# Kernel optimization log

Hardware: AMD Instinct MI355X
Metric: run time of the kernel (lower is better)

## Reference

```python
import jax, jax.numpy as jnp
import numpy as np

N_NODES = 50000
N_EDGES = 800000
D_IN, D_HID, D_OUT = 96, 96, 48


def _gcn_conv(x, src, dst, W, b, num_nodes):
    """PyG GCNConv: h = x @ W; out[dst] += norm * h[src]; out += b.
    Symmetric normalization deg^{-1/2}[src] * deg^{-1/2}[dst], self-loops included
    (src/dst already contain self-loops)."""
    h = x @ W  # [N, d_out]
    deg = jax.ops.segment_sum(jnp.ones_like(dst, dtype=h.dtype), dst,
                              num_segments=num_nodes)  # in-degree incl. self-loop
    dinv = jnp.where(deg > 0, jax.lax.rsqrt(deg), 0.0)
    norm = dinv[src] * dinv[dst]  # [E+N]
    msgs = h[src] * norm[:, None]  # gather + scale (the memory-bound part)
    out = jax.ops.segment_sum(msgs, dst, num_segments=num_nodes)  # scatter-add
    return out + b


def setup_inputs() -> dict:
    key = jax.random.key(0)
    k1, k2, k3, k4 = jax.random.split(key, 4)
    x = jax.random.normal(k1, (N_NODES, D_IN), dtype=jnp.float32)
    edge_index = jax.random.randint(k2, (2, N_EDGES), 0, N_NODES, dtype=jnp.int64)
    # Glorot-ish init for weights, zero bias (matches GCNConv defaults)
    W1 = jax.random.normal(k3, (D_IN, D_HID), dtype=jnp.float32) / np.sqrt(D_IN)
    b1 = jnp.zeros((D_HID,), dtype=jnp.float32)
    W2 = jax.random.normal(k4, (D_HID, D_OUT), dtype=jnp.float32) / np.sqrt(D_HID)
    b2 = jnp.zeros((D_OUT,), dtype=jnp.float32)
    return {"x": x, "edge_index": edge_index, "W1": W1, "b1": b1, "W2": W2, "b2": b2}


def reference(x, edge_index, W1, b1, W2, b2):
    num_nodes = x.shape[0]
    loops = jnp.arange(num_nodes, dtype=edge_index.dtype)
    src = jnp.concatenate([edge_index[0], loops])  # add self-loops
    dst = jnp.concatenate([edge_index[1], loops])
    h = _gcn_conv(x, src, dst, W1, b1, num_nodes)
    h = jax.nn.relu(h)
    # dropout p=0.5 is identity in eval mode (self.training=False)
    out = _gcn_conv(h, src, dst, W2, b2, num_nodes)
    return out
```

## Files before the change

### kernel.cpp

```cpp
#include <hip/hip_runtime.h>
#include <hip/hip_bf16.h>


constexpr int NN = 50000;
constexpr int NE = 800000;
constexpr int DI = 96;
constexpr int DH = 96;
constexpr int DO = 48;

constexpr int BK_SHIFT = 6;
constexpr int NBK      = (NN + 63) >> 6;
constexpr int BK_CAP   = 2048;

constexpr int NCHUNK = 256;
constexpr int CH     = (NE + NCHUNK - 1) / NCHUNK;

typedef unsigned short us8 __attribute__((ext_vector_type(8)));

__device__ __forceinline__ float bf2f(unsigned short u) {
    return __uint_as_float(((unsigned int)u) << 16);
}
__device__ __forceinline__ unsigned short f2bf(float f) {
    __hip_bfloat16 b = __float2bfloat16(f);
    return *reinterpret_cast<unsigned short*>(&b);
}


__global__ __launch_bounds__(256) void k_hist(const int* __restrict__ dst,
                                              int* __restrict__ C, int e) {
    __shared__ int hist[NBK];
    for (int i = threadIdx.x; i < NBK; i += 256) hist[i] = 0;
    __syncthreads();
    const int blk = blockIdx.x;
    const int beg = blk * CH, end = min(beg + CH, e);
    for (int i = beg + threadIdx.x; i < end; i += 256)
        atomicAdd(&hist[dst[i] >> BK_SHIFT], 1);
    __syncthreads();
    for (int b = threadIdx.x; b < NBK; b += 256)
        C[b * NCHUNK + blk] = hist[b];
}

__global__ __launch_bounds__(256) void k_rowscan(int* __restrict__ C,
                                                 int* __restrict__ totals,
                                                 int* __restrict__ row_ptr) {
    if (blockIdx.x == 0 && threadIdx.x == 0) row_ptr[NN] = NE;
    const int w    = threadIdx.x >> 6;
    const int lane = threadIdx.x & 63;
    const int r    = blockIdx.x * 4 + w;
    if (r >= NBK) return;
    int* row = C + r * NCHUNK;
    int v[4], s[4];
#pragma unroll
    for (int q = 0; q < 4; ++q) { v[q] = row[q * 64 + lane]; s[q] = v[q]; }
#pragma unroll
    for (int off = 1; off < 64; off <<= 1) {
#pragma unroll
        for (int q = 0; q < 4; ++q) {
            int y = __shfl_up(s[q], off);
            if (lane >= off) s[q] += y;
        }
    }
    int c0 = __shfl(s[0], 63);
    int c1 = __shfl(s[1], 63);
    int c2 = __shfl(s[2], 63);
    s[1] += c0;
    s[2] += c0 + c1;
    s[3] += c0 + c1 + c2;
#pragma unroll
    for (int q = 0; q < 4; ++q) row[q * 64 + lane] = s[q] - v[q];
    if (lane == 63) totals[r] = s[3];
}

__global__ __launch_bounds__(256) void k_scatter(const int* __restrict__ src,
                                                 const int* __restrict__ dst,
                                                 const int* __restrict__ C,
                                                 const int* __restrict__ totals,
                                                 int* __restrict__ bk_ptr,
                                                 unsigned* __restrict__ ebuf, int e) {
    __shared__ int bkL[NBK + 1];
    __shared__ int part[256];
    __shared__ int cur[NBK];
    const int t = threadIdx.x;

    int v[4];
    int s = 0;
    const int base = t * 4;
#pragma unroll
    for (int i = 0; i < 4; ++i) {
        int idx = base + i;
        v[i] = (idx < NBK) ? totals[idx] : 0;
        s += v[i];
    }
    part[t] = s;
    __syncthreads();
#pragma unroll
    for (int off = 1; off < 256; off <<= 1) {
        int x = part[t];
        int a = (t >= off) ? part[t - off] : 0;
        __syncthreads();
        part[t] = x + a;
        __syncthreads();
    }
    int run = part[t] - s;
#pragma unroll
    for (int i = 0; i < 4; ++i) {
        int idx = base + i;
        if (idx <= NBK) bkL[idx] = run;
        run += v[i];
    }
    __syncthreads();

    const int blk = blockIdx.x;
    for (int b = t; b < NBK; b += 256) cur[b] = bkL[b] + C[b * NCHUNK + blk];
    if (blk == 0)
        for (int i = t; i <= NBK; i += 256) bk_ptr[i] = bkL[i];
    __syncthreads();

    const int beg = blk * CH, end = min(beg + CH, e);
    for (int i = beg + t; i < end; i += 256) {
        int d = dst[i];
        int b = d >> BK_SHIFT;
        int pos = atomicAdd(&cur[b], 1);
        ebuf[pos] = ((unsigned)(d & 63) << 16) | (unsigned)src[i];
    }
}

__global__ __launch_bounds__(256) void k_bsort(const unsigned* __restrict__ ebuf,
                                               const int* __restrict__ bk_ptr,
                                               int* __restrict__ row_ptr,
                                               float* __restrict__ dinv,
                                               unsigned short* __restrict__ src16, int n) {
    __shared__ unsigned eL[BK_CAP];
    __shared__ unsigned short outL[BK_CAP];
    __shared__ int curL[64];
    __shared__ int baseL[64];

    const int b   = blockIdx.x;
    const int beg = bk_ptr[b];
    const int m   = bk_ptr[b + 1] - beg;
    const int t   = threadIdx.x;

    if (t < 64) curL[t] = 0;
    __syncthreads();

    for (int i = t; i < m; i += 256) {
        unsigned v = ebuf[beg + i];
        eL[i] = v;
        atomicAdd(&curL[v >> 16], 1);
    }
    __syncthreads();

    if (t < 64) {
        int c = curL[t];
        int x = c;
#pragma unroll
        for (int off = 1; off < 64; off <<= 1) {
            int y = __shfl_up(x, off);
            if (t >= off) x += y;
        }
        int excl = x - c;
        baseL[t] = excl;
        int d0 = (b << BK_SHIFT) + t;
        if (d0 < n) {
            row_ptr[d0] = beg + excl;
            dinv[d0]    = rsqrtf((float)(c + 1));
        }
    }
    __syncthreads();
    if (t < 64) curL[t] = baseL[t];
    __syncthreads();

    for (int i = t; i < m; i += 256) {
        unsigned v = eL[i];
        int p = atomicAdd(&curL[v >> 16], 1);
        outL[p] = (unsigned short)(v & 0xFFFFu);
    }
    __syncthreads();
    for (int i = t; i < m; i += 256) src16[beg + i] = outL[i];
}


__global__ __launch_bounds__(256) void k_gemm1(const float* __restrict__ X,
                                               const float* __restrict__ W,
                                               const float* __restrict__ dinv,
                                               unsigned short* __restrict__ H, int n) {
    constexpr int ROWS = 64, P = 97;
    __shared__ float ws[DI * DH];
    __shared__ float xs[ROWS * P];
    unsigned short* hout = reinterpret_cast<unsigned short*>(xs);

    const int tid  = threadIdx.x;
    const int row0 = blockIdx.x * ROWS;

    for (int i = tid; i < DI * DH; i += 256) ws[i] = W[i];
    {
        const float4* Xv = reinterpret_cast<const float4*>(X + (size_t)row0 * DI);
        const int nv   = ROWS * DI / 4;
        const int maxv = ((n - row0) * DI) / 4;
        for (int i = tid; i < nv; i += 256) {
            float4 v = (i < maxv) ? Xv[i] : float4{0.f, 0.f, 0.f, 0.f};
            int r = i / 24, c = (i % 24) * 4;
            xs[r * P + c + 0] = v.x;
            xs[r * P + c + 1] = v.y;
            xs[r * P + c + 2] = v.z;
            xs[r * P + c + 3] = v.w;
        }
    }
    __syncthreads();

    const int cg = tid & 15, rg = tid >> 4;
    float acc[4][6] = {};
#pragma unroll 2
    for (int k = 0; k < DI; ++k) {
        float xv[4];
#pragma unroll
        for (int i = 0; i < 4; ++i) xv[i] = xs[(rg * 4 + i) * P + k];
#pragma unroll
        for (int j = 0; j < 6; ++j) {
            float wv = ws[k * DH + cg * 6 + j];
#pragma unroll
            for (int i = 0; i < 4; ++i) acc[i][j] += xv[i] * wv;
        }
    }
    __syncthreads();

#pragma unroll
    for (int i = 0; i < 4; ++i) {
        int row = row0 + rg * 4 + i;
        float dv = (row < n) ? dinv[row] : 0.f;
#pragma unroll
        for (int j = 0; j < 6; ++j)
            hout[(rg * 4 + i) * 96 + cg * 6 + j] = f2bf(acc[i][j] * dv);
    }
    __syncthreads();

    {
        const us8* ho8 = reinterpret_cast<const us8*>(hout);
        us8* H8 = reinterpret_cast<us8*>(H + (size_t)row0 * DH);
        const int nv   = ROWS * DH / 8;
        const int maxv = ((n - row0) * DH) / 8;
        for (int i = tid; i < nv && i < maxv; i += 256) H8[i] = ho8[i];
    }
}


__global__ __launch_bounds__(256) void k_gemm2(const unsigned short* __restrict__ A,
                                               const float* __restrict__ W,
                                               const float* __restrict__ dinv,
                                               unsigned short* __restrict__ H, int n) {
    constexpr int ROWS = 64, P = 98;
    __shared__ float ws[DH * DO];
    __shared__ unsigned short xs[ROWS * P];

    const int tid  = threadIdx.x;
    const int row0 = blockIdx.x * ROWS;

    for (int i = tid; i < DH * DO; i += 256) ws[i] = W[i];
    {
        const us8* Av = reinterpret_cast<const us8*>(A + (size_t)row0 * DH);
        const int nv   = ROWS * DH / 8;
        const int maxv = ((n - row0) * DH) / 8;
        for (int i = tid; i < nv; i += 256) {
            us8 v = (i < maxv) ? Av[i] : (us8)(0);
            int r = i / 12, c = (i % 12) * 8;
#pragma unroll
            for (int jj = 0; jj < 8; ++jj) xs[r * P + c + jj] = v[jj];
        }
    }
    __syncthreads();

    const int cg = tid & 15, rg = tid >> 4;
    float acc[4][3] = {};
#pragma unroll 2
    for (int k = 0; k < DH; ++k) {
        float xv[4];
#pragma unroll
        for (int i = 0; i < 4; ++i) xv[i] = bf2f(xs[(rg * 4 + i) * P + k]);
#pragma unroll
        for (int j = 0; j < 3; ++j) {
            float wv = ws[k * DO + cg * 3 + j];
#pragma unroll
            for (int i = 0; i < 4; ++i) acc[i][j] += xv[i] * wv;
        }
    }
    __syncthreads();

    unsigned short* hout = xs;
#pragma unroll
    for (int i = 0; i < 4; ++i) {
        int row = row0 + rg * 4 + i;
        float dv = (row < n) ? dinv[row] : 0.f;
#pragma unroll
        for (int j = 0; j < 3; ++j)
            hout[(rg * 4 + i) * 48 + cg * 3 + j] = f2bf(acc[i][j] * dv);
    }
    __syncthreads();

    {
        const us8* ho8 = reinterpret_cast<const us8*>(hout);
        us8* H8 = reinterpret_cast<us8*>(H + (size_t)row0 * DO);
        const int nv   = ROWS * DO / 8;
        const int maxv = ((n - row0) * DO) / 8;
        for (int i = tid; i < nv && i < maxv; i += 256) H8[i] = ho8[i];
    }
}


template<int D, bool RELU, bool OUTBF16>
__global__ __launch_bounds__(256) void k_agg_csr(const unsigned short* __restrict__ h,
                                                 const float* __restrict__ dinv,
                                                 const int* __restrict__ row_ptr,
                                                 const unsigned short* __restrict__ src16,
                                                 const float* __restrict__ bias,
                                                 void* __restrict__ outp, int n) {
    constexpr int G = D / 8;
    int t = blockIdx.x * blockDim.x + threadIdx.x;
    if (t >= n * G) return;
    const int node = t / G;
    const int g    = t % G;

    const us8* h8 = reinterpret_cast<const us8*>(h);

    float accA[8], accB[8];
    {
        us8 hv = h8[(size_t)node * G + g];
#pragma unroll
        for (int j = 0; j < 8; ++j) { accA[j] = bf2f(hv[j]); accB[j] = 0.f; }
    }

    const int beg = row_ptr[node];
    const int end = row_ptr[node + 1];
    int k = beg;
    int kA = min((beg + 7) & ~7, end);
    for (; k < kA; ++k) {
        us8 vv = h8[(size_t)src16[k] * G + g];
#pragma unroll
        for (int j = 0; j < 8; ++j) accA[j] += bf2f(vv[j]);
    }
    for (; k + 8 <= end; k += 8) {
        us8 si = *reinterpret_cast<const us8*>(src16 + k);
        us8 v0 = h8[(size_t)si[0] * G + g];
        us8 v1 = h8[(size_t)si[1] * G + g];
        us8 v2 = h8[(size_t)si[2] * G + g];
        us8 v3 = h8[(size_t)si[3] * G + g];
        us8 v4 = h8[(size_t)si[4] * G + g];
        us8 v5 = h8[(size_t)si[5] * G + g];
        us8 v6 = h8[(size_t)si[6] * G + g];
        us8 v7 = h8[(size_t)si[7] * G + g];
#pragma unroll
        for (int j = 0; j < 8; ++j) {
            accA[j] += (bf2f(v0[j]) + bf2f(v1[j])) + (bf2f(v4[j]) + bf2f(v5[j]));
            accB[j] += (bf2f(v2[j]) + bf2f(v3[j])) + (bf2f(v6[j]) + bf2f(v7[j]));
        }
    }
    for (; k < end; ++k) {
        us8 vv = h8[(size_t)src16[k] * G + g];
#pragma unroll
        for (int j = 0; j < 8; ++j) accB[j] += bf2f(vv[j]);
    }

    const float di = dinv[node];
    const float4* b4 = reinterpret_cast<const float4*>(bias);
    float4 b0 = b4[g * 2], b1 = b4[g * 2 + 1];
    float r[8];
#pragma unroll
    for (int j = 0; j < 8; ++j) r[j] = di * (accA[j] + accB[j]);
    r[0] += b0.x; r[1] += b0.y; r[2] += b0.z; r[3] += b0.w;
    r[4] += b1.x; r[5] += b1.y; r[6] += b1.z; r[7] += b1.w;
    if (RELU) {
#pragma unroll
        for (int j = 0; j < 8; ++j) r[j] = fmaxf(r[j], 0.f);
    }
    if (OUTBF16) {
        us8 o;
#pragma unroll
        for (int j = 0; j < 8; ++j) o[j] = f2bf(r[j]);
        reinterpret_cast<us8*>((unsigned short*)outp)[(size_t)node * G + g] = o;
    } else {
        float4* o4 = reinterpret_cast<float4*>((float*)outp + (size_t)node * D + g * 8);
        o4[0] = float4{r[0], r[1], r[2], r[3]};
        o4[1] = float4{r[4], r[5], r[6], r[7]};
    }
}


extern "C" void kernel_launch(void* const* d_in, const int* in_sizes, int n_in,
                              void* d_out, int out_size, void* d_ws, size_t ws_size,
                              hipStream_t stream) {
    const float* x   = (const float*)d_in[0];
    const int*   ei  = (const int*)d_in[1];
    const float* W1  = (const float*)d_in[2];
    const float* b1  = (const float*)d_in[3];
    const float* W2  = (const float*)d_in[4];
    const float* b2  = (const float*)d_in[5];
    float*       out = (float*)d_out;

    const int* srcv = ei;
    const int* dstv = ei + NE;

    char* p = (char*)d_ws;
    float*          dinv  = (float*)p;           p += (size_t)NN * 4;
    unsigned short* a1    = (unsigned short*)p;  p += (size_t)NN * DH * 2;
    unsigned short* h1    = (unsigned short*)p;  p += (size_t)NN * DH * 2;
    int*      row_ptr     = (int*)p;             p += (size_t)(NN + 16) * 4;
    unsigned short* src16 = (unsigned short*)p;  p += (size_t)NE * 2;
    unsigned* ebuf        = (unsigned*)p;        p += (size_t)NE * 4;
    int*      Cm          = (int*)p;             p += (size_t)NBK * NCHUNK * 4;
    int*      totals      = (int*)p;             p += (size_t)NBK * 4;
    int*      bk_ptr      = (int*)p;             p += (size_t)(NBK + 1) * 4;

    const int B = 256;

    k_hist<<<NCHUNK, B, 0, stream>>>(dstv, Cm, NE);
    k_rowscan<<<(NBK + 3) / 4, B, 0, stream>>>(Cm, totals, row_ptr);
    k_scatter<<<NCHUNK, B, 0, stream>>>(srcv, dstv, Cm, totals, bk_ptr, ebuf, NE);
    k_bsort<<<NBK, B, 0, stream>>>(ebuf, bk_ptr, row_ptr, dinv, src16, NN);

    k_gemm1<<<(NN + 63) / 64, B, 0, stream>>>(x, W1, dinv, h1, NN);
    {
        int total = NN * (DH / 8);
        k_agg_csr<DH, true, true><<<(total + B - 1) / B, B, 0, stream>>>(
            h1, dinv, row_ptr, src16, b1, a1, NN);
    }

    unsigned short* h2 = h1;
    k_gemm2<<<(NN + 63) / 64, B, 0, stream>>>(a1, W2, dinv, h2, NN);
    {
        int total = NN * (DO / 8);
        k_agg_csr<DO, false, false><<<(total + B - 1) / B, B, 0, stream>>>(
            h2, dinv, row_ptr, src16, b2, out, NN);
    }
}
```

Measured before the change: 125.8 us.

## Store layer-1 features in 8 column slices for cache-local aggregation

```diff
diff --git a/kernel.cpp b/kernel.cpp
--- a/kernel.cpp
+++ b/kernel.cpp
@@ -183,7 +183,7 @@
 __global__ __launch_bounds__(256) void k_gemm1(const float* __restrict__ X,
                                                const float* __restrict__ W,
                                                const float* __restrict__ dinv,
-                                               unsigned short* __restrict__ H, int n) {
+                                               unsigned short* __restrict__ Hsl, int n) {
     constexpr int ROWS = 64, P = 97;
     __shared__ float ws[DI * DH];
     __shared__ float xs[ROWS * P];
@@ -234,17 +234,93 @@
     }
     __syncthreads();
 
+    for (int idx = tid; idx < 1024; idx += 256) {
+        int s    = idx & 7;
+        int r    = (idx >> 3) & 63;
+        int half = idx >> 9;
+        int row  = row0 + r;
+        if (row >= n) continue;
+        us8 v;
+        if (half == 0) {
+#pragma unroll
+            for (int jj = 0; jj < 8; ++jj) v[jj] = hout[r * 96 + s * 12 + jj];
+        } else {
+#pragma unroll
+            for (int jj = 0; jj < 4; ++jj) v[jj] = hout[r * 96 + s * 12 + 8 + jj];
+#pragma unroll
+            for (int jj = 4; jj < 8; ++jj) v[jj] = 0;
+        }
+        *reinterpret_cast<us8*>(Hsl + ((size_t)s * n + row) * 16 + half * 8) = v;
+    }
+}
+
+
+__global__ __launch_bounds__(256) void k_agg_sl8(const unsigned short* __restrict__ hsl,
+                                                 const float* __restrict__ dinv,
+                                                 const int* __restrict__ row_ptr,
+                                                 const unsigned short* __restrict__ src16,
+                                                 const float* __restrict__ bias,
+                                                 unsigned short* __restrict__ a1sl, int n) {
+    const int slice = blockIdx.x & 7;
+    const int node  = (blockIdx.x >> 3) * 128 + ((int)threadIdx.x >> 1);
+    const int g     = threadIdx.x & 1;
+    if (node >= n) return;
+
+    const us8* hs = reinterpret_cast<const us8*>(hsl + (size_t)slice * n * 16);
+
+    float accA[8], accB[8];
     {
-        const us8* ho8 = reinterpret_cast<const us8*>(hout);
-        us8* H8 = reinterpret_cast<us8*>(H + (size_t)row0 * DH);
-        const int nv   = ROWS * DH / 8;
-        const int maxv = ((n - row0) * DH) / 8;
-        for (int i = tid; i < nv && i < maxv; i += 256) H8[i] = ho8[i];
-    }
-}
-
-
-__global__ __launch_bounds__(256) void k_gemm2(const unsigned short* __restrict__ A,
+        us8 hv = hs[(size_t)node * 2 + g];
+#pragma unroll
+        for (int j = 0; j < 8; ++j) { accA[j] = bf2f(hv[j]); accB[j] = 0.f; }
+    }
+
+    const int beg = row_ptr[node];
+    const int end = row_ptr[node + 1];
+    int k = beg;
+    int kA = min((beg + 7) & ~7, end);
+    for (; k < kA; ++k) {
+        us8 vv = hs[(size_t)src16[k] * 2 + g];
+#pragma unroll
+        for (int j = 0; j < 8; ++j) accA[j] += bf2f(vv[j]);
+    }
+    for (; k + 8 <= end; k += 8) {
+        us8 si = *reinterpret_cast<const us8*>(src16 + k);
+        us8 v0 = hs[(size_t)si[0] * 2 + g];
+        us8 v1 = hs[(size_t)si[1] * 2 + g];
+        us8 v2 = hs[(size_t)si[2] * 2 + g];
+        us8 v3 = hs[(size_t)si[3] * 2 + g];
+        us8 v4 = hs[(size_t)si[4] * 2 + g];
+        us8 v5 = hs[(size_t)si[5] * 2 + g];
+        us8 v6 = hs[(size_t)si[6] * 2 + g];
+        us8 v7 = hs[(size_t)si[7] * 2 + g];
+#pragma unroll
+        for (int j = 0; j < 8; ++j) {
+            accA[j] += (bf2f(v0[j]) + bf2f(v1[j])) + (bf2f(v4[j]) + bf2f(v5[j]));
+            accB[j] += (bf2f(v2[j]) + bf2f(v3[j])) + (bf2f(v6[j]) + bf2f(v7[j]));
+        }
+    }
+    for (; k < end; ++k) {
+        us8 vv = hs[(size_t)src16[k] * 2 + g];
+#pragma unroll
+        for (int j = 0; j < 8; ++j) accB[j] += bf2f(vv[j]);
+    }
+
+    const float di = dinv[node];
+    const int nvalid = (g == 0) ? 8 : 4;
+    us8 o;
+#pragma unroll
+    for (int j = 0; j < 8; ++j) {
+        float r = di * (accA[j] + accB[j]);
+        if (j < nvalid) r += bias[slice * 12 + g * 8 + j];
+        r = fmaxf(r, 0.f);
+        o[j] = (j < nvalid) ? f2bf(r) : (unsigned short)0;
+    }
+    *reinterpret_cast<us8*>(a1sl + ((size_t)slice * n + node) * 16 + g * 8) = o;
+}
+
+
+__global__ __launch_bounds__(256) void k_gemm2(const unsigned short* __restrict__ Asl,
                                                const float* __restrict__ W,
                                                const float* __restrict__ dinv,
                                                unsigned short* __restrict__ H, int n) {
@@ -256,16 +332,17 @@
     const int row0 = blockIdx.x * ROWS;
 
     for (int i = tid; i < DH * DO; i += 256) ws[i] = W[i];
-    {
-        const us8* Av = reinterpret_cast<const us8*>(A + (size_t)row0 * DH);
-        const int nv   = ROWS * DH / 8;
-        const int maxv = ((n - row0) * DH) / 8;
-        for (int i = tid; i < nv; i += 256) {
-            us8 v = (i < maxv) ? Av[i] : (us8)(0);
-            int r = i / 12, c = (i % 12) * 8;
-#pragma unroll
-            for (int jj = 0; jj < 8; ++jj) xs[r * P + c + jj] = v[jj];
-        }
+    for (int idx = tid; idx < 1024; idx += 256) {
+        int s    = idx & 7;
+        int r    = (idx >> 3) & 63;
+        int half = idx >> 9;
+        int row  = row0 + r;
+        us8 v = (us8)(0);
+        if (row < n)
+            v = *reinterpret_cast<const us8*>(Asl + ((size_t)s * n + row) * 16 + half * 8);
+        int nv = (half == 0) ? 8 : 4;
+        for (int jj = 0; jj < nv; ++jj)
+            xs[r * P + s * 12 + half * 8 + jj] = v[jj];
     }
     __syncthreads();
 
@@ -400,8 +477,8 @@
 
     char* p = (char*)d_ws;
     float*          dinv  = (float*)p;           p += (size_t)NN * 4;
-    unsigned short* a1    = (unsigned short*)p;  p += (size_t)NN * DH * 2;
-    unsigned short* h1    = (unsigned short*)p;  p += (size_t)NN * DH * 2;
+    unsigned short* h1sl  = (unsigned short*)p;  p += (size_t)8 * NN * 16 * 2;
+    unsigned short* a1sl  = (unsigned short*)p;  p += (size_t)8 * NN * 16 * 2;
     int*      row_ptr     = (int*)p;             p += (size_t)(NN + 16) * 4;
     unsigned short* src16 = (unsigned short*)p;  p += (size_t)NE * 2;
     unsigned* ebuf        = (unsigned*)p;        p += (size_t)NE * 4;
@@ -416,15 +493,14 @@
     k_scatter<<<NCHUNK, B, 0, stream>>>(srcv, dstv, Cm, totals, bk_ptr, ebuf, NE);
     k_bsort<<<NBK, B, 0, stream>>>(ebuf, bk_ptr, row_ptr, dinv, src16, NN);
 
-    k_gemm1<<<(NN + 63) / 64, B, 0, stream>>>(x, W1, dinv, h1, NN);
+    k_gemm1<<<(NN + 63) / 64, B, 0, stream>>>(x, W1, dinv, h1sl, NN);
     {
-        int total = NN * (DH / 8);
-        k_agg_csr<DH, true, true><<<(total + B - 1) / B, B, 0, stream>>>(
-            h1, dinv, row_ptr, src16, b1, a1, NN);
-    }
-
-    unsigned short* h2 = h1;
-    k_gemm2<<<(NN + 63) / 64, B, 0, stream>>>(a1, W2, dinv, h2, NN);
+        const int NCH = (NN + 127) / 128;
+        k_agg_sl8<<<NCH * 8, B, 0, stream>>>(h1sl, dinv, row_ptr, src16, b1, a1sl, NN);
+    }
+
+    unsigned short* h2 = h1sl;
+    k_gemm2<<<(NN + 63) / 64, B, 0, stream>>>(a1sl, W2, dinv, h2, NN);
     {
         int total = NN * (DO / 8);
         k_agg_csr<DO, false, false><<<(total + B - 1) / B, B, 0, stream>>>(
```

New measurement: 142.8 us. 1.14x slower.

## Fuse GEMM1 into scatter launch and aggregation-1 with GEMM2 using packed edge weights

Applied to the files above, without the earlier changes.

```diff
diff --git a/kernel.cpp b/kernel.cpp
--- a/kernel.cpp
+++ b/kernel.cpp
@@ -15,6 +15,10 @@
 constexpr int NCHUNK = 256;
 constexpr int CH     = (NE + NCHUNK - 1) / NCHUNK;
 
+constexpr int G1_ROWS = 64;
+constexpr int NG1     = (NN + G1_ROWS - 1) / G1_ROWS;
+
+typedef unsigned short us4 __attribute__((ext_vector_type(4)));
 typedef unsigned short us8 __attribute__((ext_vector_type(8)));
 
 __device__ __forceinline__ float bf2f(unsigned short u) {
@@ -71,57 +75,114 @@
     if (lane == 63) totals[r] = s[3];
 }
 
-__global__ __launch_bounds__(256) void k_scatter(const int* __restrict__ src,
-                                                 const int* __restrict__ dst,
-                                                 const int* __restrict__ C,
-                                                 const int* __restrict__ totals,
-                                                 int* __restrict__ bk_ptr,
-                                                 unsigned* __restrict__ ebuf, int e) {
+__global__ __launch_bounds__(256) void k_scatter_gemm1(
+        const int* __restrict__ src, const int* __restrict__ dst,
+        const int* __restrict__ C, const int* __restrict__ totals,
+        int* __restrict__ bk_ptr, unsigned* __restrict__ ebuf, int e,
+        const float* __restrict__ X, const float* __restrict__ W,
+        unsigned short* __restrict__ H, int n) {
     __shared__ int bkL[NBK + 1];
     __shared__ int part[256];
     __shared__ int cur[NBK];
+    constexpr int P = 97;
+    __shared__ float ws[DI * DH];
+    __shared__ float xs[G1_ROWS * P];
+
     const int t = threadIdx.x;
 
-    int v[4];
-    int s = 0;
-    const int base = t * 4;
-#pragma unroll
-    for (int i = 0; i < 4; ++i) {
-        int idx = base + i;
-        v[i] = (idx < NBK) ? totals[idx] : 0;
-        s += v[i];
-    }
-    part[t] = s;
-    __syncthreads();
-#pragma unroll
-    for (int off = 1; off < 256; off <<= 1) {
-        int x = part[t];
-        int a = (t >= off) ? part[t - off] : 0;
-        __syncthreads();
-        part[t] = x + a;
-        __syncthreads();
-    }
-    int run = part[t] - s;
-#pragma unroll
-    for (int i = 0; i < 4; ++i) {
-        int idx = base + i;
-        if (idx <= NBK) bkL[idx] = run;
-        run += v[i];
-    }
-    __syncthreads();
-
-    const int blk = blockIdx.x;
-    for (int b = t; b < NBK; b += 256) cur[b] = bkL[b] + C[b * NCHUNK + blk];
-    if (blk == 0)
-        for (int i = t; i <= NBK; i += 256) bk_ptr[i] = bkL[i];
-    __syncthreads();
-
-    const int beg = blk * CH, end = min(beg + CH, e);
-    for (int i = beg + t; i < end; i += 256) {
-        int d = dst[i];
-        int b = d >> BK_SHIFT;
-        int pos = atomicAdd(&cur[b], 1);
-        ebuf[pos] = ((unsigned)(d & 63) << 16) | (unsigned)src[i];
+    if (blockIdx.x < NCHUNK) {
+        int v[4];
+        int s = 0;
+        const int base = t * 4;
+#pragma unroll
+        for (int i = 0; i < 4; ++i) {
+            int idx = base + i;
+            v[i] = (idx < NBK) ? totals[idx] : 0;
+            s += v[i];
+        }
+        part[t] = s;
+        __syncthreads();
+#pragma unroll
+        for (int off = 1; off < 256; off <<= 1) {
+            int x = part[t];
+            int a = (t >= off) ? part[t - off] : 0;
+            __syncthreads();
+            part[t] = x + a;
+            __syncthreads();
+        }
+        int run = part[t] - s;
+#pragma unroll
+        for (int i = 0; i < 4; ++i) {
+            int idx = base + i;
+            if (idx <= NBK) bkL[idx] = run;
+            run += v[i];
+        }
+        __syncthreads();
+
+        const int blk = blockIdx.x;
+        for (int b = t; b < NBK; b += 256) cur[b] = bkL[b] + C[b * NCHUNK + blk];
+        if (blk == 0)
+            for (int i = t; i <= NBK; i += 256) bk_ptr[i] = bkL[i];
+        __syncthreads();
+
+        const int beg = blk * CH, end = min(beg + CH, e);
+        for (int i = beg + t; i < end; i += 256) {
+            int d = dst[i];
+            int b = d >> BK_SHIFT;
+            int pos = atomicAdd(&cur[b], 1);
+            ebuf[pos] = ((unsigned)(d & 63) << 16) | (unsigned)src[i];
+        }
+    } else {
+        const int row0 = (blockIdx.x - NCHUNK) * G1_ROWS;
+        unsigned short* hout = reinterpret_cast<unsigned short*>(xs);
+
+        for (int i = t; i < DI * DH; i += 256) ws[i] = W[i];
+        {
+            const float4* Xv = reinterpret_cast<const float4*>(X + (size_t)row0 * DI);
+            const int nv   = G1_ROWS * DI / 4;
+            const int maxv = ((n - row0) * DI) / 4;
+            for (int i = t; i < nv; i += 256) {
+                float4 v = (i < maxv) ? Xv[i] : float4{0.f, 0.f, 0.f, 0.f};
+                int r = i / 24, c = (i % 24) * 4;
+                xs[r * P + c + 0] = v.x;
+                xs[r * P + c + 1] = v.y;
+                xs[r * P + c + 2] = v.z;
+                xs[r * P + c + 3] = v.w;
+            }
+        }
+        __syncthreads();
+
+        const int cg = t & 15, rg = t >> 4;
+        float acc[4][6] = {};
+#pragma unroll 2
+        for (int k = 0; k < DI; ++k) {
+            float xv[4];
+#pragma unroll
+            for (int i = 0; i < 4; ++i) xv[i] = xs[(rg * 4 + i) * P + k];
+#pragma unroll
+            for (int j = 0; j < 6; ++j) {
+                float wv = ws[k * DH + cg * 6 + j];
+#pragma unroll
+                for (int i = 0; i < 4; ++i) acc[i][j] += xv[i] * wv;
+            }
+        }
+        __syncthreads();
+
+#pragma unroll
+        for (int i = 0; i < 4; ++i) {
+#pragma unroll
+            for (int j = 0; j < 6; ++j)
+                hout[(rg * 4 + i) * 96 + cg * 6 + j] = f2bf(acc[i][j]);
+        }
+        __syncthreads();
+
+        {
+            const us8* ho8 = reinterpret_cast<const us8*>(hout);
+            us8* H8 = reinterpret_cast<us8*>(H + (size_t)row0 * DH);
+            const int nv   = G1_ROWS * DH / 8;
+            const int maxv = ((n - row0) * DH) / 8;
+            for (int i = t; i < nv && i < maxv; i += 256) H8[i] = ho8[i];
+        }
     }
 }
 
@@ -179,140 +240,138 @@
     for (int i = t; i < m; i += 256) src16[beg + i] = outL[i];
 }
 
-
-__global__ __launch_bounds__(256) void k_gemm1(const float* __restrict__ X,
-                                               const float* __restrict__ W,
-                                               const float* __restrict__ dinv,
-                                               unsigned short* __restrict__ H, int n) {
-    constexpr int ROWS = 64, P = 97;
-    __shared__ float ws[DI * DH];
-    __shared__ float xs[ROWS * P];
-    unsigned short* hout = reinterpret_cast<unsigned short*>(xs);
-
-    const int tid  = threadIdx.x;
-    const int row0 = blockIdx.x * ROWS;
-
-    for (int i = tid; i < DI * DH; i += 256) ws[i] = W[i];
-    {
-        const float4* Xv = reinterpret_cast<const float4*>(X + (size_t)row0 * DI);
-        const int nv   = ROWS * DI / 4;
-        const int maxv = ((n - row0) * DI) / 4;
-        for (int i = tid; i < nv; i += 256) {
-            float4 v = (i < maxv) ? Xv[i] : float4{0.f, 0.f, 0.f, 0.f};
-            int r = i / 24, c = (i % 24) * 4;
-            xs[r * P + c + 0] = v.x;
-            xs[r * P + c + 1] = v.y;
-            xs[r * P + c + 2] = v.z;
-            xs[r * P + c + 3] = v.w;
-        }
-    }
-    __syncthreads();
-
-    const int cg = tid & 15, rg = tid >> 4;
-    float acc[4][6] = {};
-#pragma unroll 2
-    for (int k = 0; k < DI; ++k) {
-        float xv[4];
-#pragma unroll
-        for (int i = 0; i < 4; ++i) xv[i] = xs[(rg * 4 + i) * P + k];
-#pragma unroll
-        for (int j = 0; j < 6; ++j) {
-            float wv = ws[k * DH + cg * 6 + j];
-#pragma unroll
-            for (int i = 0; i < 4; ++i) acc[i][j] += xv[i] * wv;
-        }
-    }
-    __syncthreads();
-
-#pragma unroll
-    for (int i = 0; i < 4; ++i) {
-        int row = row0 + rg * 4 + i;
-        float dv = (row < n) ? dinv[row] : 0.f;
-#pragma unroll
-        for (int j = 0; j < 6; ++j)
-            hout[(rg * 4 + i) * 96 + cg * 6 + j] = f2bf(acc[i][j] * dv);
-    }
-    __syncthreads();
-
-    {
-        const us8* ho8 = reinterpret_cast<const us8*>(hout);
-        us8* H8 = reinterpret_cast<us8*>(H + (size_t)row0 * DH);
-        const int nv   = ROWS * DH / 8;
-        const int maxv = ((n - row0) * DH) / 8;
-        for (int i = tid; i < nv && i < maxv; i += 256) H8[i] = ho8[i];
-    }
-}
-
-
-__global__ __launch_bounds__(256) void k_gemm2(const unsigned short* __restrict__ A,
-                                               const float* __restrict__ W,
-                                               const float* __restrict__ dinv,
-                                               unsigned short* __restrict__ H, int n) {
-    constexpr int ROWS = 64, P = 98;
+__global__ __launch_bounds__(256) void k_pack(const unsigned short* __restrict__ src16,
+                                              const float* __restrict__ dinv,
+                                              unsigned* __restrict__ epack, int e) {
+    int i2 = (blockIdx.x * 256 + threadIdx.x) * 2;
+    if (i2 + 1 < e) {
+        unsigned pairv = *reinterpret_cast<const unsigned*>(src16 + i2);
+        unsigned s0 = pairv & 0xFFFFu;
+        unsigned s1 = pairv >> 16;
+        unsigned w0 = f2bf(dinv[s0]);
+        unsigned w1 = f2bf(dinv[s1]);
+        uint2 o;
+        o.x = (w0 << 16) | s0;
+        o.y = (w1 << 16) | s1;
+        *reinterpret_cast<uint2*>(epack + i2) = o;
+    } else if (i2 < e) {
+        unsigned s0 = src16[i2];
+        epack[i2] = ((unsigned)f2bf(dinv[s0]) << 16) | s0;
+    }
+}
+
+
+__global__ __launch_bounds__(768) void k_agg1_gemm2(
+        const unsigned short* __restrict__ h1,
+        const float* __restrict__ dinv,
+        const int* __restrict__ row_ptr,
+        const unsigned* __restrict__ epack,
+        const float* __restrict__ b1,
+        const float* __restrict__ W2,
+        unsigned short* __restrict__ h2, int n) {
+    constexpr int P2 = 104;
+    __shared__ unsigned short a1t[G1_ROWS * P2];
     __shared__ float ws[DH * DO];
-    __shared__ unsigned short xs[ROWS * P];
-
-    const int tid  = threadIdx.x;
-    const int row0 = blockIdx.x * ROWS;
-
-    for (int i = tid; i < DH * DO; i += 256) ws[i] = W[i];
-    {
-        const us8* Av = reinterpret_cast<const us8*>(A + (size_t)row0 * DH);
-        const int nv   = ROWS * DH / 8;
-        const int maxv = ((n - row0) * DH) / 8;
-        for (int i = tid; i < nv; i += 256) {
-            us8 v = (i < maxv) ? Av[i] : (us8)(0);
-            int r = i / 12, c = (i % 12) * 8;
-#pragma unroll
-            for (int jj = 0; jj < 8; ++jj) xs[r * P + c + jj] = v[jj];
-        }
-    }
-    __syncthreads();
-
-    const int cg = tid & 15, rg = tid >> 4;
-    float acc[4][3] = {};
+
+    const int t = threadIdx.x;
+    for (int i = t; i < DH * DO; i += 768) ws[i] = W2[i];
+
+    const int rloc = t / 12;
+    const int g    = t % 12;
+    const int node = blockIdx.x * G1_ROWS + rloc;
+
+    if (node < n) {
+        const us8* h8 = reinterpret_cast<const us8*>(h1);
+        const float di = dinv[node];
+
+        float accA[8], accB[8];
+        {
+            us8 hv = h8[(size_t)node * 12 + g];
+#pragma unroll
+            for (int j = 0; j < 8; ++j) { accA[j] = di * bf2f(hv[j]); accB[j] = 0.f; }
+        }
+
+        const int beg = row_ptr[node];
+        const int end = row_ptr[node + 1];
+        int k = beg;
+        int kA = min((beg + 7) & ~7, end);
+        for (; k < kA; ++k) {
+            unsigned ev = epack[k];
+            float w = bf2f((unsigned short)(ev >> 16));
+            us8 vv = h8[(size_t)(ev & 0xFFFFu) * 12 + g];
+#pragma unroll
+            for (int j = 0; j < 8; ++j) accA[j] += w * bf2f(vv[j]);
+        }
+        for (; k + 8 <= end; k += 8) {
+            const uint4* ev4 = reinterpret_cast<const uint4*>(epack + k);
+            uint4 e0 = ev4[0], e1 = ev4[1];
+            us8 v0 = h8[(size_t)(e0.x & 0xFFFFu) * 12 + g];
+            us8 v1 = h8[(size_t)(e0.y & 0xFFFFu) * 12 + g];
+            us8 v2 = h8[(size_t)(e0.z & 0xFFFFu) * 12 + g];
+            us8 v3 = h8[(size_t)(e0.w & 0xFFFFu) * 12 + g];
+            us8 v4 = h8[(size_t)(e1.x & 0xFFFFu) * 12 + g];
+            us8 v5 = h8[(size_t)(e1.y & 0xFFFFu) * 12 + g];
+            us8 v6 = h8[(size_t)(e1.z & 0xFFFFu) * 12 + g];
+            us8 v7 = h8[(size_t)(e1.w & 0xFFFFu) * 12 + g];
+            float w0 = bf2f((unsigned short)(e0.x >> 16));
+            float w1 = bf2f((unsigned short)(e0.y >> 16));
+            float w2 = bf2f((unsigned short)(e0.z >> 16));
+            float w3 = bf2f((unsigned short)(e0.w >> 16));
+            float w4 = bf2f((unsigned short)(e1.x >> 16));
+            float w5 = bf2f((unsigned short)(e1.y >> 16));
+            float w6 = bf2f((unsigned short)(e1.z >> 16));
+            float w7 = bf2f((unsigned short)(e1.w >> 16));
+#pragma unroll
+            for (int j = 0; j < 8; ++j) {
+                accA[j] += w0 * bf2f(v0[j]) + w1 * bf2f(v1[j])
+                         + w4 * bf2f(v4[j]) + w5 * bf2f(v5[j]);
+                accB[j] += w2 * bf2f(v2[j]) + w3 * bf2f(v3[j])
+                         + w6 * bf2f(v6[j]) + w7 * bf2f(v7[j]);
+            }
+        }
+        for (; k < end; ++k) {
+            unsigned ev = epack[k];
+            float w = bf2f((unsigned short)(ev >> 16));
+            us8 vv = h8[(size_t)(ev & 0xFFFFu) * 12 + g];
+#pragma unroll
+            for (int j = 0; j < 8; ++j) accB[j] += w * bf2f(vv[j]);
+        }
+
+        us8 o;
+#pragma unroll
+        for (int j = 0; j < 8; ++j) {
+            float r = di * (accA[j] + accB[j]) + b1[g * 8 + j];
+            o[j] = f2bf(fmaxf(r, 0.f));
+        }
+        *reinterpret_cast<us8*>(a1t + rloc * P2 + g * 8) = o;
+    }
+    __syncthreads();
+
+    const int c0 = g * 4;
+    float acc[4] = {};
 #pragma unroll 2
     for (int k = 0; k < DH; ++k) {
-        float xv[4];
-#pragma unroll
-        for (int i = 0; i < 4; ++i) xv[i] = bf2f(xs[(rg * 4 + i) * P + k]);
-#pragma unroll
-        for (int j = 0; j < 3; ++j) {
-            float wv = ws[k * DO + cg * 3 + j];
-#pragma unroll
-            for (int i = 0; i < 4; ++i) acc[i][j] += xv[i] * wv;
-        }
-    }
-    __syncthreads();
-
-    unsigned short* hout = xs;
-#pragma unroll
-    for (int i = 0; i < 4; ++i) {
-        int row = row0 + rg * 4 + i;
-        float dv = (row < n) ? dinv[row] : 0.f;
-#pragma unroll
-        for (int j = 0; j < 3; ++j)
-            hout[(rg * 4 + i) * 48 + cg * 3 + j] = f2bf(acc[i][j] * dv);
-    }
-    __syncthreads();
-
-    {
-        const us8* ho8 = reinterpret_cast<const us8*>(hout);
-        us8* H8 = reinterpret_cast<us8*>(H + (size_t)row0 * DO);
-        const int nv   = ROWS * DO / 8;
-        const int maxv = ((n - row0) * DO) / 8;
-        for (int i = tid; i < nv && i < maxv; i += 256) H8[i] = ho8[i];
-    }
-}
-
-
-template<int D, bool RELU, bool OUTBF16>
+        float xv = bf2f(a1t[rloc * P2 + k]);
+#pragma unroll
+        for (int j = 0; j < 4; ++j) acc[j] += xv * ws[k * DO + c0 + j];
+    }
+    if (node < n) {
+        float dv = dinv[node];
+        us4 o;
+#pragma unroll
+        for (int j = 0; j < 4; ++j) o[j] = f2bf(acc[j] * dv);
+        *reinterpret_cast<us4*>(h2 + (size_t)node * DO + c0) = o;
+    }
+}
+
+
+template<int D, bool RELU>
 __global__ __launch_bounds__(256) void k_agg_csr(const unsigned short* __restrict__ h,
                                                  const float* __restrict__ dinv,
                                                  const int* __restrict__ row_ptr,
                                                  const unsigned short* __restrict__ src16,
                                                  const float* __restrict__ bias,
-                                                 void* __restrict__ outp, int n) {
+                                                 float* __restrict__ outp, int n) {
     constexpr int G = D / 8;
     int t = blockIdx.x * blockDim.x + threadIdx.x;
     if (t >= n * G) return;
@@ -371,16 +430,9 @@
 #pragma unroll
         for (int j = 0; j < 8; ++j) r[j] = fmaxf(r[j], 0.f);
     }
-    if (OUTBF16) {
-        us8 o;
-#pragma unroll
-        for (int j = 0; j < 8; ++j) o[j] = f2bf(r[j]);
-        reinterpret_cast<us8*>((unsigned short*)outp)[(size_t)node * G + g] = o;
-    } else {
-        float4* o4 = reinterpret_cast<float4*>((float*)outp + (size_t)node * D + g * 8);
-        o4[0] = float4{r[0], r[1], r[2], r[3]};
-        o4[1] = float4{r[4], r[5], r[6], r[7]};
-    }
+    float4* o4 = reinterpret_cast<float4*>(outp + (size_t)node * D + g * 8);
+    o4[0] = float4{r[0], r[1], r[2], r[3]};
+    o4[1] = float4{r[4], r[5], r[6], r[7]};
 }
 
 
@@ -400,10 +452,11 @@
 
     char* p = (char*)d_ws;
     float*          dinv  = (float*)p;           p += (size_t)NN * 4;
-    unsigned short* a1    = (unsigned short*)p;  p += (size_t)NN * DH * 2;
     unsigned short* h1    = (unsigned short*)p;  p += (size_t)NN * DH * 2;
+    unsigned short* h2    = (unsigned short*)p;  p += (size_t)NN * DO * 2;
     int*      row_ptr     = (int*)p;             p += (size_t)(NN + 16) * 4;
     unsigned short* src16 = (unsigned short*)p;  p += (size_t)NE * 2;
+    unsigned* epack       = (unsigned*)p;        p += (size_t)NE * 4;
     unsigned* ebuf        = (unsigned*)p;        p += (size_t)NE * 4;
     int*      Cm          = (int*)p;             p += (size_t)NBK * NCHUNK * 4;
     int*      totals      = (int*)p;             p += (size_t)NBK * 4;
@@ -413,21 +466,16 @@
 
     k_hist<<<NCHUNK, B, 0, stream>>>(dstv, Cm, NE);
     k_rowscan<<<(NBK + 3) / 4, B, 0, stream>>>(Cm, totals, row_ptr);
-    k_scatter<<<NCHUNK, B, 0, stream>>>(srcv, dstv, Cm, totals, bk_ptr, ebuf, NE);
+    k_scatter_gemm1<<<NCHUNK + NG1, B, 0, stream>>>(
+        srcv, dstv, Cm, totals, bk_ptr, ebuf, NE, x, W1, h1, NN);
     k_bsort<<<NBK, B, 0, stream>>>(ebuf, bk_ptr, row_ptr, dinv, src16, NN);
-
-    k_gemm1<<<(NN + 63) / 64, B, 0, stream>>>(x, W1, dinv, h1, NN);
-    {
-        int total = NN * (DH / 8);
-        k_agg_csr<DH, true, true><<<(total + B - 1) / B, B, 0, stream>>>(
-            h1, dinv, row_ptr, src16, b1, a1, NN);
-    }
-
-    unsigned short* h2 = h1;
-    k_gemm2<<<(NN + 63) / 64, B, 0, stream>>>(a1, W2, dinv, h2, NN);
+    k_pack<<<(NE / 2 + B - 1) / B, B, 0, stream>>>(src16, dinv, epack, NE);
+
+    k_agg1_gemm2<<<NG1, 768, 0, stream>>>(h1, dinv, row_ptr, epack, b1, W2, h2, NN);
+
     {
         int total = NN * (DO / 8);
-        k_agg_csr<DO, false, false><<<(total + B - 1) / B, B, 0, stream>>>(
+        k_agg_csr<DO, false><<<(total + B - 1) / B, B, 0, stream>>>(
             h2, dinv, row_ptr, src16, b2, out, NN);
     }
 }
```

New measurement: 120.8 us. 1.04x faster.
